# Optimization experiments

Hardware: AMD Instinct MI355X
Metric: run time of the kernel (lower is better)

The kernel has to match this reference:

```python
import jax, jax.numpy as jnp
import numpy as np

N_NODES = 8192


def _gcn_norm(edge_index, num_nodes):
    # PyG GCNConv default: add self-loops, symmetric normalization.
    src, dst = edge_index[0], edge_index[1]
    loop = jnp.arange(num_nodes, dtype=src.dtype)
    src = jnp.concatenate([src, loop])
    dst = jnp.concatenate([dst, loop])
    deg = jax.ops.segment_sum(jnp.ones_like(dst, dtype=jnp.float32), dst,
                              num_segments=num_nodes)
    dis = jnp.where(deg > 0, jax.lax.rsqrt(jnp.maximum(deg, 1.0)), 0.0)
    norm = dis[src] * dis[dst]  # [E + N]
    return src, dst, norm


def _gcn_conv(x, W, b, src, dst, norm, num_nodes):
    h = x @ W                           # [N, F_out] dense GEMM
    msg = h[src] * norm[:, None]        # gather + scale, [E+N, F_out]
    out = jax.ops.segment_sum(msg, dst, num_segments=num_nodes)  # scatter-add
    return out + b


def setup_inputs() -> dict:
    key = jax.random.key(0)
    ks = jax.random.split(key, 8)
    N, E, F_in, H1, H2, F_out = N_NODES, 65536, 512, 4096, 1024, 10
    x = jax.random.normal(ks[0], (N, F_in), dtype=jnp.float32)
    edge_index = jax.random.randint(ks[1], (2, E), 0, N, dtype=jnp.int64)
    # Glorot-ish scaled weights
    W1 = jax.random.normal(ks[2], (F_in, H1), dtype=jnp.float32) * (1.0 / np.sqrt(F_in))
    b1 = jnp.zeros((H1,), dtype=jnp.float32)
    W2 = jax.random.normal(ks[3], (H1, H2), dtype=jnp.float32) * (1.0 / np.sqrt(H1))
    b2 = jnp.zeros((H2,), dtype=jnp.float32)
    W3 = jax.random.normal(ks[4], (H2, F_out), dtype=jnp.float32) * (1.0 / np.sqrt(H2))
    b3 = jnp.zeros((F_out,), dtype=jnp.float32)
    return {"x": x, "W1": W1, "b1": b1, "W2": W2, "b2": b2,
            "W3": W3, "b3": b3, "edge_index": edge_index}


def reference(x, W1, b1, W2, b2, W3, b3, edge_index):
    N = N_NODES
    src, dst, norm = _gcn_norm(edge_index, N)
    h = _gcn_conv(x.astype(jnp.float32), W1, b1, src, dst, norm, N)
    h = jax.nn.relu(h)  # dropout is identity in eval mode
    h = _gcn_conv(h, W2, b2, src, dst, norm, N)
    h = jax.nn.relu(h)
    h = _gcn_conv(h, W3, b3, src, dst, norm, N)
    return jax.nn.log_softmax(h, axis=1)
```

## Files before the change

### kernel.cpp

```cpp
#include <hip/hip_runtime.h>
#include <math.h>

#define N_NODES 8192
#define N_EDGES 65536
#define F_IN    512
#define HID1    4096
#define HID2    1024
#define F_OUT   10
#define H3_STRIDE 16
#define W3B_STRIDE 1032

typedef __bf16 bf16x8 __attribute__((ext_vector_type(8)));
typedef float floatx4 __attribute__((ext_vector_type(4)));
typedef float floatx16 __attribute__((ext_vector_type(16)));

static __device__ __forceinline__ unsigned short f2bf(float f) {
    union { float f; unsigned u; } v; v.f = f;
    unsigned r = v.u + 0x7fffu + ((v.u >> 16) & 1u);
    return (unsigned short)(r >> 16);
}
static __device__ __forceinline__ float bf2f(unsigned short u) {
    union { unsigned u; float f; } v; v.u = ((unsigned)u) << 16;
    return v.f;
}
static __device__ __forceinline__ void unpack8(uint4 r, float* f) {
    union { unsigned u; float v; } c;
    c.u = r.x << 16;          f[0] = c.v;
    c.u = r.x & 0xffff0000u;  f[1] = c.v;
    c.u = r.y << 16;          f[2] = c.v;
    c.u = r.y & 0xffff0000u;  f[3] = c.v;
    c.u = r.z << 16;          f[4] = c.v;
    c.u = r.z & 0xffff0000u;  f[5] = c.v;
    c.u = r.w << 16;          f[6] = c.v;
    c.u = r.w & 0xffff0000u;  f[7] = c.v;
}
static __device__ __forceinline__ uint4 pack8(const float* f) {
    uint4 o;
    o.x = (unsigned)f2bf(f[0]) | ((unsigned)f2bf(f[1]) << 16);
    o.y = (unsigned)f2bf(f[2]) | ((unsigned)f2bf(f[3]) << 16);
    o.z = (unsigned)f2bf(f[4]) | ((unsigned)f2bf(f[5]) << 16);
    o.w = (unsigned)f2bf(f[6]) | ((unsigned)f2bf(f[7]) << 16);
    return o;
}

__global__ __launch_bounds__(256) void hist_kernel(
        const int* __restrict__ ei, int* __restrict__ deg) {
    int e = blockIdx.x * 256 + threadIdx.x;
    atomicAdd(&deg[ei[N_EDGES + e]], 1);
}

__global__ __launch_bounds__(1024) void scan_kernel(
        const int* __restrict__ deg, int* __restrict__ row_ptr,
        int* __restrict__ cnt) {
    __shared__ int sums[1024];
    int t = threadIdx.x;
    int base = t * 8;
    int4 d0 = ((const int4*)deg)[t * 2];
    int4 d1 = ((const int4*)deg)[t * 2 + 1];
    int dv[8] = {d0.x, d0.y, d0.z, d0.w, d1.x, d1.y, d1.z, d1.w};
    int local[8], run = 0;
#pragma unroll
    for (int i = 0; i < 8; i++) { local[i] = run; run += dv[i]; }
    sums[t] = run;
    ((int4*)cnt)[t * 2] = make_int4(0, 0, 0, 0);
    ((int4*)cnt)[t * 2 + 1] = make_int4(0, 0, 0, 0);
    __syncthreads();
    for (int off = 1; off < 1024; off <<= 1) {
        int val = (t >= off) ? sums[t - off] : 0;
        __syncthreads();
        sums[t] += val;
        __syncthreads();
    }
    int offset = (t == 0) ? 0 : sums[t - 1];
#pragma unroll
    for (int i = 0; i < 8; i++) row_ptr[base + i] = offset + local[i];
    if (t == 1023) row_ptr[N_NODES] = sums[1023];
}

static __device__ __forceinline__ void transpose_body(
        const float* __restrict__ W, unsigned short* __restrict__ Wt,
        int K, int N, int k0, int n0, int tid, float (*t)[33]) {
    int c = tid & 31, r8 = tid >> 5;
#pragma unroll
    for (int i = 0; i < 4; i++) {
        int r = r8 + i * 8;
        t[r][c] = W[(size_t)(k0 + r) * N + n0 + c];
    }
    __syncthreads();
#pragma unroll
    for (int i = 0; i < 4; i++) {
        int r = r8 + i * 8;
        Wt[(size_t)(n0 + r) * K + k0 + c] = f2bf(t[c][r]);
    }
}

__global__ __launch_bounds__(256) void megaprep_kernel(
        const int* __restrict__ ei, const int* __restrict__ deg,
        const int* __restrict__ row_ptr, int* __restrict__ cnt,
        int* __restrict__ csr_src, float* __restrict__ csr_w,
        const float* __restrict__ x, unsigned short* __restrict__ xb,
        const float* __restrict__ W1, unsigned short* __restrict__ W1t,
        const float* __restrict__ W2, unsigned short* __restrict__ W2t,
        const float* __restrict__ W3, unsigned short* __restrict__ w3b) {
    __shared__ float t[32][33];
    int b = blockIdx.x, tid = threadIdx.x;
    if (b < 256) {
        int e = b * 256 + tid;
        int s = ei[e];
        int d = ei[N_EDGES + e];
        int slot = row_ptr[d] + atomicAdd(&cnt[d], 1);
        csr_src[slot] = s;
        csr_w[slot] = rsqrtf((float)((deg[s] + 1) * (deg[d] + 1)));
    } else if (b < 4352) {
        int i = (b - 256) * 256 + tid;
        float4 a = ((const float4*)x)[i];
        ushort4 o;
        o.x = f2bf(a.x); o.y = f2bf(a.y); o.z = f2bf(a.z); o.w = f2bf(a.w);
        ((ushort4*)xb)[i] = o;
    } else if (b < 6400) {
        int bb = b - 4352;
        transpose_body(W1, W1t, F_IN, HID1, (bb >> 7) * 32, (bb & 127) * 32, tid, t);
    } else if (b < 10496) {
        int bb = b - 6400;
        transpose_body(W2, W2t, HID1, HID2, (bb >> 5) * 32, (bb & 31) * 32, tid, t);
    } else {
        for (int i = tid; i < HID2 * F_OUT; i += 256) {
            int k = i / F_OUT, c = i % F_OUT;
            w3b[c * W3B_STRIDE + k] = f2bf(W3[i]);
        }
    }
}

__global__ __launch_bounds__(256) void agg1_kernel(
        const unsigned short* __restrict__ xb, const int* __restrict__ row_ptr,
        const int* __restrict__ csr_src, const float* __restrict__ csr_w,
        const int* __restrict__ deg, unsigned short* __restrict__ out) {
    int v = blockIdx.x * 4 + (threadIdx.x >> 6);
    int t = threadIdx.x & 63;
    const uint4* xp = (const uint4*)xb;
    float sw = 1.0f / (float)(deg[v] + 1);
    float acc[8], tmp[8];
    unpack8(xp[(size_t)v * 64 + t], tmp);
#pragma unroll
    for (int j = 0; j < 8; j++) acc[j] = sw * tmp[j];
    int e = row_ptr[v], end = row_ptr[v + 1];
    for (; e + 4 <= end; e += 4) {
        int s0 = csr_src[e], s1 = csr_src[e + 1];
        int s2 = csr_src[e + 2], s3 = csr_src[e + 3];
        float w0 = csr_w[e], w1 = csr_w[e + 1];
        float w2 = csr_w[e + 2], w3 = csr_w[e + 3];
        float f0[8], f1[8], f2[8], f3[8];
        unpack8(xp[(size_t)s0 * 64 + t], f0);
        unpack8(xp[(size_t)s1 * 64 + t], f1);
        unpack8(xp[(size_t)s2 * 64 + t], f2);
        unpack8(xp[(size_t)s3 * 64 + t], f3);
#pragma unroll
        for (int j = 0; j < 8; j++)
            acc[j] += w0 * f0[j] + w1 * f1[j] + w2 * f2[j] + w3 * f3[j];
    }
    for (; e < end; e++) {
        int s = csr_src[e];
        float w = csr_w[e];
        float f0[8];
        unpack8(xp[(size_t)s * 64 + t], f0);
#pragma unroll
        for (int j = 0; j < 8; j++) acc[j] += w * f0[j];
    }
    ((uint4*)out)[(size_t)v * 64 + t] = pack8(acc);
}

__global__ __launch_bounds__(256) void agg2_gemm3_kernel(
        const unsigned short* __restrict__ h, const int* __restrict__ row_ptr,
        const int* __restrict__ csr_src, const float* __restrict__ csr_w,
        const int* __restrict__ deg, const float* __restrict__ b2,
        const unsigned short* __restrict__ w3b, float* __restrict__ H3) {
    __shared__ unsigned short w3s[F_OUT * W3B_STRIDE];
    __shared__ float red[4][F_OUT];
    int tid = threadIdx.x;
    for (int i = tid; i < F_OUT * W3B_STRIDE; i += 256) w3s[i] = w3b[i];
    __syncthreads();
    int half = tid >> 7;
    int t = tid & 127;
    int v = blockIdx.x * 2 + half;
    const uint4* hp = (const uint4*)h;
    float sw = 1.0f / (float)(deg[v] + 1);
    float acc[8], tmp[8];
    unpack8(hp[(size_t)v * 128 + t], tmp);
#pragma unroll
    for (int j = 0; j < 8; j++) acc[j] = sw * tmp[j];
    int e = row_ptr[v], end = row_ptr[v + 1];
    for (; e + 4 <= end; e += 4) {
        int s0 = csr_src[e], s1 = csr_src[e + 1];
        int s2 = csr_src[e + 2], s3 = csr_src[e + 3];
        float w0 = csr_w[e], w1 = csr_w[e + 1];
        float w2 = csr_w[e + 2], w3 = csr_w[e + 3];
        float f0[8], f1[8], f2[8], f3[8];
        unpack8(hp[(size_t)s0 * 128 + t], f0);
        unpack8(hp[(size_t)s1 * 128 + t], f1);
        unpack8(hp[(size_t)s2 * 128 + t], f2);
        unpack8(hp[(size_t)s3 * 128 + t], f3);
#pragma unroll
        for (int j = 0; j < 8; j++)
            acc[j] += w0 * f0[j] + w1 * f1[j] + w2 * f2[j] + w3 * f3[j];
    }
    for (; e < end; e++) {
        int s = csr_src[e];
        float w = csr_w[e];
        float f0[8];
        unpack8(hp[(size_t)s * 128 + t], f0);
#pragma unroll
        for (int j = 0; j < 8; j++) acc[j] += w * f0[j];
    }
    float4 b4a = ((const float4*)b2)[t * 2];
    float4 b4b = ((const float4*)b2)[t * 2 + 1];
    acc[0] = fmaxf(acc[0] + b4a.x, 0.0f); acc[1] = fmaxf(acc[1] + b4a.y, 0.0f);
    acc[2] = fmaxf(acc[2] + b4a.z, 0.0f); acc[3] = fmaxf(acc[3] + b4a.w, 0.0f);
    acc[4] = fmaxf(acc[4] + b4b.x, 0.0f); acc[5] = fmaxf(acc[5] + b4b.y, 0.0f);
    acc[6] = fmaxf(acc[6] + b4b.z, 0.0f); acc[7] = fmaxf(acc[7] + b4b.w, 0.0f);

    float partial[F_OUT];
#pragma unroll
    for (int c = 0; c < F_OUT; c++) {
        float wf[8];
        unpack8(*(const uint4*)&w3s[c * W3B_STRIDE + t * 8], wf);
        partial[c] = acc[0] * wf[0] + acc[1] * wf[1] + acc[2] * wf[2] + acc[3] * wf[3]
                   + acc[4] * wf[4] + acc[5] * wf[5] + acc[6] * wf[6] + acc[7] * wf[7];
    }
#pragma unroll
    for (int c = 0; c < F_OUT; c++) {
#pragma unroll
        for (int off = 32; off > 0; off >>= 1)
            partial[c] += __shfl_xor(partial[c], off, 64);
    }
    int wave = tid >> 6, lane = tid & 63;
    if (lane == 0) {
#pragma unroll
        for (int c = 0; c < F_OUT; c++) red[wave][c] = partial[c];
    }
    __syncthreads();
    if (tid < 2 * F_OUT) {
        int hh = tid / F_OUT, c = tid % F_OUT;
        H3[(size_t)(blockIdx.x * 2 + hh) * H3_STRIDE + c] =
            red[hh * 2][c] + red[hh * 2 + 1][c];
    }
}

#define P8_OFF(R_, lc_) ((((R_) >> 2) * 128) + (((((R_) & 3) << 2) | (lc_)) ^ (((R_) >> 2) & 3)) * 8)

#define Q4_STAGE(Lbuf_, base_, k0_) do {                                       \
    unsigned short* L_ = (Lbuf_);                                              \
    _Pragma("unroll")                                                          \
    for (int j = 0; j < 2; j++) {                                              \
        int sl = j * 512 + tid;                                                \
        int s4 = sl >> 4, cs = sl & 15;                                        \
        int csp = cs ^ (s4 & 3);                                               \
        int grow = s4 * 4 + (csp >> 2);                                        \
        int gcol = (csp & 3) * 8;                                              \
        __builtin_amdgcn_global_load_lds(                                      \
            (const __attribute__((address_space(1))) void*)((base_) + (size_t)grow * K + (k0_) + gcol), \
            (__attribute__((address_space(3))) void*)(&L_[sl * 8]), 16, 0, 0); \
    }                                                                          \
} while (0)

#define P8_STAGE(mat_, kh_, dd_, base_, k0_) \
    Q4_STAGE(lds + ((dd_) * 4 + (mat_) * 2 + (kh_)) * 8192, base_, (k0_) + (kh_) * 32)

#define P8_MAIN_LOOP(NT_)                                                      \
    P8_STAGE(0, 0, 0, Abase, 0);                                               \
    P8_STAGE(1, 0, 0, Bbase, 0);                                               \
    P8_STAGE(0, 1, 0, Abase, 0);                                               \
    P8_STAGE(1, 1, 0, Bbase, 0);                                               \
    asm volatile("s_waitcnt vmcnt(4)" ::: "memory");                           \
    __builtin_amdgcn_s_barrier();                                              \
    for (int t = 0; t < (NT_); t++) {                                          \
        int d = t & 1, dn = d ^ 1;                                             \
        int k1 = (t + 1) * 64;                                                 \
        _Pragma("unroll")                                                      \
        for (int kk = 0; kk < 4; kk++) {                                       \
            if (kk == 2) {                                                     \
                if (t + 1 < (NT_))                                             \
                    asm volatile("s_waitcnt vmcnt(4)" ::: "memory");           \
                else                                                           \
                    asm volatile("s_waitcnt vmcnt(0)" ::: "memory");           \
                __builtin_amdgcn_s_barrier();                                  \
            }                                                                  \
            int kh = kk >> 1;                                                  \
            int lc0 = (kk & 1) * 2 + lhalf;                                    \
            const unsigned short* Ak = lds + (d * 4 + kh) * 8192;              \
            const unsigned short* Bk = lds + (d * 4 + 2 + kh) * 8192;          \
            bf16x8 af[4], bfr[2];                                              \
            _Pragma("unroll")                                                  \
            for (int mt = 0; mt < 4; mt++) {                                   \
                int R = wm * 128 + mt * 32 + lrow;                             \
                af[mt] = *(const bf16x8*)&Ak[P8_OFF(R, lc0)];                  \
            }                                                                  \
            _Pragma("unroll")                                                  \
            for (int nt = 0; nt < 2; nt++) {                                   \
                int R = wn * 64 + nt * 32 + lrow;                              \
                bfr[nt] = *(const bf16x8*)&Bk[P8_OFF(R, lc0)];                 \
            }                                                                  \
            if (t + 1 < (NT_)) {                                               \
                if (kk == 0)      P8_STAGE(0, 0, dn, Abase, k1);               \
                else if (kk == 1) P8_STAGE(1, 0, dn, Bbase, k1);               \
                else if (kk == 2) P8_STAGE(0, 1, dn, Abase, k1);               \
                else              P8_STAGE(1, 1, dn, Bbase, k1);               \
            }                                                                  \
            __builtin_amdgcn_s_barrier();                                      \
            __builtin_amdgcn_s_setprio(1);                                     \
            _Pragma("unroll")                                                  \
            for (int mt = 0; mt < 4; mt++)                                     \
                _Pragma("unroll")                                              \
                for (int nt = 0; nt < 2; nt++)                                 \
                    acc[mt][nt] = __builtin_amdgcn_mfma_f32_32x32x16_bf16(     \
                        af[mt], bfr[nt], acc[mt][nt], 0, 0, 0);                \
            __builtin_amdgcn_s_setprio(0);                                     \
            if (kk == 0 || kk == 2) __builtin_amdgcn_s_barrier();              \
        }                                                                      \
        asm volatile("s_waitcnt vmcnt(4)" ::: "memory");                       \
        __builtin_amdgcn_s_barrier();                                          \
    }

__global__ __launch_bounds__(512, 2) void gemm1_pipe8_kernel(
        const unsigned short* __restrict__ A,
        const unsigned short* __restrict__ Bt,
        const float* __restrict__ bias,
        unsigned short* __restrict__ C) {
    __shared__ unsigned short lds[65536];
    const int K = F_IN, N = HID1;
    int tid = threadIdx.x;
    int wave = tid >> 6, lane = tid & 63;
    int wm = wave >> 2, wn = wave & 3;
    int lrow = lane & 31, lhalf = lane >> 5;

    int b = blockIdx.x;
    int GN = HID1 >> 8;
    int ntile = (b >> 3) % GN;
    int mtile = ((b >> 3) / GN) * 8 + (b & 7);
    int m0 = mtile * 256, n0 = ntile * 256;

    const unsigned short* Abase = A + (size_t)m0 * K;
    const unsigned short* Bbase = Bt + (size_t)n0 * K;

    floatx16 acc[4][2] = {};
    P8_MAIN_LOOP(8)

#pragma unroll
    for (int mt = 0; mt < 4; mt++) {
#pragma unroll
        for (int nt = 0; nt < 2; nt++) {
            int col = n0 + wn * 64 + nt * 32 + lrow;
            float bv = bias[col];
#pragma unroll
            for (int reg = 0; reg < 16; reg++) {
                int row = m0 + wm * 128 + mt * 32 + (reg & 3) + 8 * (reg >> 2) + 4 * lhalf;
                float v = fmaxf(acc[mt][nt][reg] + bv, 0.0f);
                C[(size_t)row * N + col] = f2bf(v);
            }
        }
    }
}

__global__ __launch_bounds__(512, 2) void gemm2_q4_split_kernel(
        const unsigned short* __restrict__ A,
        const unsigned short* __restrict__ Bt,
        unsigned short* __restrict__ Ca,
        unsigned short* __restrict__ Cb) {
    __shared__ unsigned short lds[65536];
    const int K = HID1;
    const int N = HID2;
    int tid = threadIdx.x;
    int wave = tid >> 6, lane = tid & 63;
    int wm = wave >> 2, wn = wave & 3;
    int lrow = lane & 31, lhalf = lane >> 5;

    int b = blockIdx.x;
    int u = b >> 3;
    int col = u & 7;
    int mtile = (u >> 3) * 8 + (b & 7);
    int ntile = col >> 1;
    int ksp = col & 1;
    int m0 = mtile * 256, n0 = ntile * 256;
    int koff = ksp * (HID1 / 2);

    const unsigned short* Abase = A + (size_t)m0 * K + koff;
    const unsigned short* Bbase = Bt + (size_t)n0 * K + koff;
    unsigned short* Cout = ksp ? Cb : Ca;

    floatx16 acc[4][2] = {};
    const int NT = (HID1 / 2) >> 5;

    Q4_STAGE(lds + 0 * 16384, Abase, 0);  Q4_STAGE(lds + 0 * 16384 + 8192, Bbase, 0);
    Q4_STAGE(lds + 1 * 16384, Abase, 32); Q4_STAGE(lds + 1 * 16384 + 8192, Bbase, 32);
    Q4_STAGE(lds + 2 * 16384, Abase, 64); Q4_STAGE(lds + 2 * 16384 + 8192, Bbase, 64);
    asm volatile("s_waitcnt vmcnt(8)" ::: "memory");
    __builtin_amdgcn_s_barrier();

    for (int t = 0; t < NT; t++) {
        const unsigned short* Ak = lds + (size_t)(t & 3) * 16384;
        const unsigned short* Bk = Ak + 8192;
        unsigned short* Lnext = lds + (size_t)((t + 3) & 3) * 16384;
        int k3 = (t + 3) * 32;
#pragma unroll
        for (int kk = 0; kk < 2; kk++) {
            int lc0 = kk * 2 + lhalf;
            bf16x8 af[4], bfr[2];
#pragma unroll
            for (int mt = 0; mt < 4; mt++) {
                int R = wm * 128 + mt * 32 + lrow;
                af[mt] = *(const bf16x8*)&Ak[P8_OFF(R, lc0)];
            }
#pragma unroll
            for (int nt = 0; nt < 2; nt++) {
                int R = wn * 64 + nt * 32 + lrow;
                bfr[nt] = *(const bf16x8*)&Bk[P8_OFF(R, lc0)];
            }
            if (t + 3 < NT) {
                if (kk == 0) Q4_STAGE(Lnext, Abase, k3);
                else         Q4_STAGE(Lnext + 8192, Bbase, k3);
            }
            __builtin_amdgcn_s_setprio(1);
#pragma unroll
            for (int mt = 0; mt < 4; mt++)
#pragma unroll
                for (int nt = 0; nt < 2; nt++)
                    acc[mt][nt] = __builtin_amdgcn_mfma_f32_32x32x16_bf16(
                        af[mt], bfr[nt], acc[mt][nt], 0, 0, 0);
            __builtin_amdgcn_s_setprio(0);
        }
        if (t + 3 < NT)
            asm volatile("s_waitcnt vmcnt(8)" ::: "memory");
        else if (t + 2 < NT)
            asm volatile("s_waitcnt vmcnt(4)" ::: "memory");
        else if (t + 1 < NT)
            asm volatile("s_waitcnt vmcnt(0)" ::: "memory");
        __builtin_amdgcn_s_barrier();
    }

#pragma unroll
    for (int mt = 0; mt < 4; mt++) {
#pragma unroll
        for (int nt = 0; nt < 2; nt++) {
            int colc = n0 + wn * 64 + nt * 32 + lrow;
#pragma unroll
            for (int reg = 0; reg < 16; reg++) {
                int row = m0 + wm * 128 + mt * 32 + (reg & 3) + 8 * (reg >> 2) + 4 * lhalf;
                Cout[(size_t)row * N + colc] = f2bf(acc[mt][nt][reg]);
            }
        }
    }
}

__global__ __launch_bounds__(256) void merge_kernel(
        const unsigned short* __restrict__ Ca, unsigned short* __restrict__ Cb) {
    const uint4* a4 = (const uint4*)Ca;
    uint4* b4 = (uint4*)Cb;
    int base = blockIdx.x * 1024 + threadIdx.x;
#pragma unroll
    for (int j = 0; j < 4; j++) {
        int i = base + j * 256;
        float fa[8], fb[8];
        unpack8(a4[i], fa);
        unpack8(b4[i], fb);
#pragma unroll
        for (int k = 0; k < 8; k++) fa[k] += fb[k];
        b4[i] = pack8(fa);
    }
}

__global__ void final_kernel(const float* __restrict__ h3, const int* __restrict__ row_ptr,
                             const int* __restrict__ csr_src, const float* __restrict__ csr_w,
                             const int* __restrict__ deg, const float* __restrict__ b3,
                             float* __restrict__ out) {
    int v = blockIdx.x * blockDim.x + threadIdx.x;
    if (v >= N_NODES) return;
    const float4* h4 = (const float4*)h3;
    float sw = 1.0f / (float)(deg[v] + 1);
    float a[12];
    *(float4*)&a[0] = h4[v * 4];
    *(float4*)&a[4] = h4[v * 4 + 1];
    *(float4*)&a[8] = h4[v * 4 + 2];
    float acc[F_OUT];
#pragma unroll
    for (int c = 0; c < F_OUT; c++) acc[c] = b3[c] + sw * a[c];
    int end = row_ptr[v + 1];
    for (int e = row_ptr[v]; e < end; e++) {
        int s = csr_src[e];
        float w = csr_w[e];
        float bsrc[12];
        *(float4*)&bsrc[0] = h4[s * 4];
        *(float4*)&bsrc[4] = h4[s * 4 + 1];
        *(float4*)&bsrc[8] = h4[s * 4 + 2];
#pragma unroll
        for (int c = 0; c < F_OUT; c++) acc[c] += w * bsrc[c];
    }
    float m = acc[0];
#pragma unroll
    for (int c = 1; c < F_OUT; c++) m = fmaxf(m, acc[c]);
    float ssum = 0.0f;
#pragma unroll
    for (int c = 0; c < F_OUT; c++) ssum += expf(acc[c] - m);
    float l = logf(ssum);
#pragma unroll
    for (int c = 0; c < F_OUT; c++) out[v * F_OUT + c] = acc[c] - m - l;
}

extern "C" void kernel_launch(void* const* d_in, const int* in_sizes, int n_in,
                              void* d_out, int out_size, void* d_ws, size_t ws_size,
                              hipStream_t stream) {
    const float* x  = (const float*)d_in[0];
    const float* W1 = (const float*)d_in[1];
    const float* b1 = (const float*)d_in[2];
    const float* W2 = (const float*)d_in[3];
    const float* b2 = (const float*)d_in[4];
    const float* W3 = (const float*)d_in[5];
    const float* b3 = (const float*)d_in[6];
    const int*   ei = (const int*)d_in[7];
    float* out = (float*)d_out;

    char* p = (char*)d_ws;
    int*   deg     = (int*)p;    p += N_NODES * 4;
    int*   cnt     = (int*)p;    p += N_NODES * 4;
    int*   row_ptr = (int*)p;    p += 33024;
    int*   csr_src = (int*)p;    p += N_EDGES * 4;
    float* csr_w   = (float*)p;  p += N_EDGES * 4;
    float* h3      = (float*)p;  p += N_NODES * H3_STRIDE * 4;
    unsigned short* w3b = (unsigned short*)p; p += (F_OUT * W3B_STRIDE * 2 + 255) / 256 * 256;
    unsigned short* xb    = (unsigned short*)p; p += (size_t)N_NODES * F_IN * 2;
    unsigned short* agg_x = (unsigned short*)p; p += (size_t)N_NODES * F_IN * 2;
    unsigned short* W1t   = (unsigned short*)p; p += (size_t)HID1 * F_IN * 2;
    unsigned short* W2t   = (unsigned short*)p; p += (size_t)HID2 * HID1 * 2;
    unsigned short* h1    = (unsigned short*)p; p += (size_t)N_NODES * HID1 * 2;
    unsigned short* h2pre = (unsigned short*)p; p += (size_t)N_NODES * HID2 * 2;
    unsigned short* h2a = xb;

    hipMemsetAsync(deg, 0, N_NODES * sizeof(int), stream);
    hist_kernel<<<N_EDGES / 256, 256, 0, stream>>>(ei, deg);
    scan_kernel<<<1, 1024, 0, stream>>>(deg, row_ptr, cnt);
    megaprep_kernel<<<10497, 256, 0, stream>>>(ei, deg, row_ptr, cnt, csr_src, csr_w,
                                               x, xb, W1, W1t, W2, W2t, W3, w3b);

    agg1_kernel<<<N_NODES / 4, 256, 0, stream>>>(xb, row_ptr, csr_src, csr_w, deg, agg_x);
    gemm1_pipe8_kernel<<<(N_NODES / 256) * (HID1 / 256), 512, 0, stream>>>(
        agg_x, W1t, b1, h1);

    gemm2_q4_split_kernel<<<256, 512, 0, stream>>>(h1, W2t, h2a, h2pre);
    merge_kernel<<<1024, 256, 0, stream>>>(h2a, h2pre);

    agg2_gemm3_kernel<<<N_NODES / 2, 256, 0, stream>>>(h2pre, row_ptr, csr_src, csr_w,
                                                       deg, b2, w3b, h3);

    final_kernel<<<N_NODES / 256, 256, 0, stream>>>(h3, row_ptr, csr_src, csr_w, deg, b3, out);
}
```

Before: 289.8 us.

## Fuse histogram into scan kernel and restructure gemm2 prefetch/MFMA ordering

Replaces the memset, global-atomic histogram and scan kernels with one single-block kernel that builds the degree histogram in LDS with shared atomics and then scans it, removing two launches and global atomic traffic. In the gemm2 kernel, all global-to-LDS staging for the tile three steps ahead is issued at the top of each iteration, both k-substeps of fragments are loaded before issuing all MFMAs in one prioritized burst. This raises register pressure for fragments and puts all of the histogram on a single workgroup, which could serialize 65536 LDS atomics on one CU.

```diff
diff --git a/kernel.cpp b/kernel.cpp
--- a/kernel.cpp
+++ b/kernel.cpp
@@ -43,27 +43,35 @@
     return o;
 }
 
-__global__ __launch_bounds__(256) void hist_kernel(
-        const int* __restrict__ ei, int* __restrict__ deg) {
-    int e = blockIdx.x * 256 + threadIdx.x;
-    atomicAdd(&deg[ei[N_EDGES + e]], 1);
-}
-
-__global__ __launch_bounds__(1024) void scan_kernel(
-        const int* __restrict__ deg, int* __restrict__ row_ptr,
-        int* __restrict__ cnt) {
+__global__ __launch_bounds__(1024) void hist_scan_kernel(
+        const int* __restrict__ ei, int* __restrict__ deg,
+        int* __restrict__ row_ptr, int* __restrict__ cnt) {
+    __shared__ int hist[N_NODES];
     __shared__ int sums[1024];
     int t = threadIdx.x;
+#pragma unroll
+    for (int i = 0; i < 8; i++) hist[t + i * 1024] = 0;
+    __syncthreads();
+    const int4* ei4 = (const int4*)(ei + N_EDGES);
+#pragma unroll
+    for (int i = 0; i < 16; i++) {
+        int4 d4 = ei4[i * 1024 + t];
+        atomicAdd(&hist[d4.x], 1);
+        atomicAdd(&hist[d4.y], 1);
+        atomicAdd(&hist[d4.z], 1);
+        atomicAdd(&hist[d4.w], 1);
+    }
+    __syncthreads();
     int base = t * 8;
-    int4 d0 = ((const int4*)deg)[t * 2];
-    int4 d1 = ((const int4*)deg)[t * 2 + 1];
-    int dv[8] = {d0.x, d0.y, d0.z, d0.w, d1.x, d1.y, d1.z, d1.w};
     int local[8], run = 0;
 #pragma unroll
-    for (int i = 0; i < 8; i++) { local[i] = run; run += dv[i]; }
+    for (int i = 0; i < 8; i++) {
+        int dv = hist[base + i];
+        deg[base + i] = dv;
+        cnt[base + i] = 0;
+        local[i] = run; run += dv;
+    }
     sums[t] = run;
-    ((int4*)cnt)[t * 2] = make_int4(0, 0, 0, 0);
-    ((int4*)cnt)[t * 2 + 1] = make_int4(0, 0, 0, 0);
     __syncthreads();
     for (int off = 1; off < 1024; off <<= 1) {
         int val = (t >= off) ? sums[t - off] : 0;
@@ -360,7 +368,7 @@
     }
 }
 
-__global__ __launch_bounds__(512, 2) void gemm2_q4_split_kernel(
+__global__ __launch_bounds__(512, 2) void gemm2_q4v2_split_kernel(
         const unsigned short* __restrict__ A,
         const unsigned short* __restrict__ Bt,
         unsigned short* __restrict__ Ca,
@@ -400,33 +408,35 @@
         const unsigned short* Bk = Ak + 8192;
         unsigned short* Lnext = lds + (size_t)((t + 3) & 3) * 16384;
         int k3 = (t + 3) * 32;
+        if (t + 3 < NT) {
+            Q4_STAGE(Lnext, Abase, k3);
+            Q4_STAGE(Lnext + 8192, Bbase, k3);
+        }
+        bf16x8 af[2][4], bfr[2][2];
 #pragma unroll
         for (int kk = 0; kk < 2; kk++) {
             int lc0 = kk * 2 + lhalf;
-            bf16x8 af[4], bfr[2];
 #pragma unroll
             for (int mt = 0; mt < 4; mt++) {
                 int R = wm * 128 + mt * 32 + lrow;
-                af[mt] = *(const bf16x8*)&Ak[P8_OFF(R, lc0)];
+                af[kk][mt] = *(const bf16x8*)&Ak[P8_OFF(R, lc0)];
             }
 #pragma unroll
             for (int nt = 0; nt < 2; nt++) {
                 int R = wn * 64 + nt * 32 + lrow;
-                bfr[nt] = *(const bf16x8*)&Bk[P8_OFF(R, lc0)];
+                bfr[kk][nt] = *(const bf16x8*)&Bk[P8_OFF(R, lc0)];
             }
-            if (t + 3 < NT) {
-                if (kk == 0) Q4_STAGE(Lnext, Abase, k3);
-                else         Q4_STAGE(Lnext + 8192, Bbase, k3);
-            }
-            __builtin_amdgcn_s_setprio(1);
+        }
+        __builtin_amdgcn_s_setprio(1);
+#pragma unroll
+        for (int kk = 0; kk < 2; kk++)
 #pragma unroll
             for (int mt = 0; mt < 4; mt++)
 #pragma unroll
                 for (int nt = 0; nt < 2; nt++)
                     acc[mt][nt] = __builtin_amdgcn_mfma_f32_32x32x16_bf16(
-                        af[mt], bfr[nt], acc[mt][nt], 0, 0, 0);
-            __builtin_amdgcn_s_setprio(0);
-        }
+                        af[kk][mt], bfr[kk][nt], acc[mt][nt], 0, 0, 0);
+        __builtin_amdgcn_s_setprio(0);
         if (t + 3 < NT)
             asm volatile("s_waitcnt vmcnt(8)" ::: "memory");
         else if (t + 2 < NT)
@@ -533,9 +543,7 @@
     unsigned short* h2pre = (unsigned short*)p; p += (size_t)N_NODES * HID2 * 2;
     unsigned short* h2a = xb;
 
-    hipMemsetAsync(deg, 0, N_NODES * sizeof(int), stream);
-    hist_kernel<<<N_EDGES / 256, 256, 0, stream>>>(ei, deg);
-    scan_kernel<<<1, 1024, 0, stream>>>(deg, row_ptr, cnt);
+    hist_scan_kernel<<<1, 1024, 0, stream>>>(ei, deg, row_ptr, cnt);
     megaprep_kernel<<<10497, 256, 0, stream>>>(ei, deg, row_ptr, cnt, csr_src, csr_w,
                                                x, xb, W1, W1t, W2, W2t, W3, w3b);
 
@@ -543,7 +551,7 @@
     gemm1_pipe8_kernel<<<(N_NODES / 256) * (HID1 / 256), 512, 0, stream>>>(
         agg_x, W1t, b1, h1);
 
-    gemm2_q4_split_kernel<<<256, 512, 0, stream>>>(h1, W2t, h2a, h2pre);
+    gemm2_q4v2_split_kernel<<<256, 512, 0, stream>>>(h1, W2t, h2a, h2pre);
     merge_kernel<<<1024, 256, 0, stream>>>(h2a, h2pre);
 
     agg2_gemm3_kernel<<<N_NODES / 2, 256, 0, stream>>>(h2pre, row_ptr, csr_src, csr_w,
```

After: 287.2 us. About the same (-0.9%).
